# Performance work log

Measured on AMD Instinct MI355X. Metric: run time of the kernel, lower is better.

## Reference

```python
import jax, jax.numpy as jnp
import numpy as np

EPS = 1e-6        # eigenvalue clamp for numerical safety (matrices are well-conditioned by construction)
MOMENTUM = 0.1    # init kwarg


def _sym_apply(X, fn):
    """Apply a spectral function to a batch of symmetric matrices via eigh."""
    w, V = jnp.linalg.eigh(X)
    w = jnp.maximum(w, EPS)
    return jnp.einsum('...ij,...j,...kj->...ik', V, fn(w), V)


def sqrtm(X):
    return _sym_apply(X, jnp.sqrt)


def invsqrtm(X):
    return _sym_apply(X, lambda w: 1.0 / jnp.sqrt(w))


def logm(X):
    return _sym_apply(X, jnp.log)


def expm_sym(X):
    w, V = jnp.linalg.eigh(X)
    return jnp.einsum('...ij,...j,...kj->...ik', V, jnp.exp(w), V)


def powm(X, t):
    return _sym_apply(X, lambda w: w ** t)


def congr_neg(X, G):
    """CongrG(X, G, 'neg') = G^{-1/2} X G^{-1/2}, broadcast over batch dims of X."""
    Gi = invsqrtm(G)
    return jnp.einsum('ij,...jk,kl->...il', Gi, X, Gi)


def bary_geom(Xm):
    """Karcher (Frechet) mean of SPD matrices Xm: (N, n, n).
    One Karcher-flow step initialized at the arithmetic mean (SPDNet-BN convention)."""
    G = jnp.mean(Xm, axis=0)
    Gs, Gi = sqrtm(G), invsqrtm(G)
    L = logm(jnp.einsum('ij,bjk,kl->bil', Gi, Xm, Gi))   # log-maps at G
    return Gs @ expm_sym(jnp.mean(L, axis=0)) @ Gs


def geodesic(A, B, t):
    """SPD geodesic from A toward B at time t: A^{1/2} (A^{-1/2} B A^{-1/2})^t A^{1/2}."""
    As, Ai = sqrtm(A), invsqrtm(A)
    return As @ powm(Ai @ B @ Ai, t) @ As


def setup_inputs() -> dict:
    key = jax.random.key(0)
    N, T, V, M, n = 32, 64, 25, 2, 16
    A = jax.random.normal(key, (N, T, V, M, n, n), dtype=jnp.float32)
    # SPD construction: A A^T / n + 0.5 I  (min eigenvalue >= 0.5)
    X = jnp.einsum('...ij,...kj->...ik', A, A) / n + 0.5 * jnp.eye(n, dtype=jnp.float32)
    running_mean = jnp.eye(n, dtype=jnp.float32)  # torch.eye(n) in __init__
    return {"X": X, "running_mean": running_mean}


def reference(X, running_mean):
    N, T, V, M, n, _ = X.shape
    Xf = X.reshape(N, T * V * M, n, n)
    X_mean = jnp.mean(Xf, axis=1)                      # (N, n, n) per-sample arithmetic mean
    mean = bary_geom(X_mean)                           # (n, n) Karcher mean over batch
    new_running_mean = geodesic(running_mean, mean, MOMENTUM)  # no_grad EMA in torch
    X_centered = congr_neg(Xf, mean)                   # mean^{-1/2} X mean^{-1/2}
    return X_centered.reshape(N, T, V, M, n, n), new_running_mean
```

## Files before the change

kernel.cpp:

```cpp
#include <hip/hip_runtime.h>
#include <math.h>

#define NSAMP  32
#define BBATCH 3200
#define NMAT   102400
#define ST     20
#define IX(i,j) ((i)*ST+(j))
#define MSZ    (16*ST)

#define PART_O 0
#define WI_O   131072

#define NS_IT 5
#define LOG_M 7
#define EXP_M 6


__device__ __forceinline__ void wsync() {
  asm volatile("s_waitcnt lgkmcnt(0)" ::: "memory");
}

__device__ __forceinline__ void wmm(const float* A, const float* B, float* C, int l) {
  int i = l >> 2, j0 = (l & 3) << 2;
  float4 acc = make_float4(0.f, 0.f, 0.f, 0.f);
  #pragma unroll
  for (int k = 0; k < 16; ++k) {
    float a = A[IX(i, k)];
    const float4 b = *(const float4*)&B[IX(k, j0)];
    acc.x += a * b.x; acc.y += a * b.y; acc.z += a * b.z; acc.w += a * b.w;
  }
  *(float4*)&C[IX(i, j0)] = acc;
  wsync();
}

__device__ __forceinline__ void wmad_diag(float* C, float s, float d, int l) {
  int i = l >> 2, j0 = (l & 3) << 2;
  float4 p = *(float4*)&C[IX(i, j0)];
  p.x *= s; p.y *= s; p.z *= s; p.w *= s;
  if (i == j0) p.x += d; else if (i == j0 + 1) p.y += d;
  else if (i == j0 + 2) p.z += d; else if (i == j0 + 3) p.w += d;
  *(float4*)&C[IX(i, j0)] = p;
  wsync();
}

__device__ __forceinline__ void wset_I(float* C, float d, int l) {
  int i = l >> 2, j0 = (l & 3) << 2;
  float4 p = make_float4(0.f, 0.f, 0.f, 0.f);
  if (i == j0) p.x = d; else if (i == j0 + 1) p.y = d;
  else if (i == j0 + 2) p.z = d; else if (i == j0 + 3) p.w = d;
  *(float4*)&C[IX(i, j0)] = p;
  wsync();
}

__device__ __forceinline__ void wsym(float* A, int l) {
  int i = l >> 2, j0 = (l & 3) << 2;
  float4 a = *(float4*)&A[IX(i, j0)];
  float4 v;
  v.x = 0.5f * (a.x + A[IX(j0,     i)]);
  v.y = 0.5f * (a.y + A[IX(j0 + 1, i)]);
  v.z = 0.5f * (a.z + A[IX(j0 + 2, i)]);
  v.w = 0.5f * (a.w + A[IX(j0 + 3, i)]);
  wsync();
  *(float4*)&A[IX(i, j0)] = v;
  wsync();
}

__device__ __forceinline__ float wtrace(const float* A) {
  float tr = 0.f;
  #pragma unroll
  for (int k = 0; k < 16; ++k) tr += A[IX(k, k)];
  return tr;
}

__device__ __forceinline__ void wcpy(const float* src, float* dst, int l) {
  int i = l >> 2, j0 = (l & 3) << 2;
  *(float4*)&dst[IX(i, j0)] = *(const float4*)&src[IX(i, j0)];
  wsync();
}

__device__ void wns(float* Y0, float* Y1, float* Z0, float* Z1, float* P,
                    int l, float** pS, float** pZ) {
  float c = wtrace(Y0) * (1.f / 16.f);
  float ic = 1.f / c;
  int i = l >> 2, j0 = (l & 3) << 2;
  {
    float4 a = *(float4*)&Y0[IX(i, j0)];
    a.x *= ic; a.y *= ic; a.z *= ic; a.w *= ic;
    *(float4*)&Y0[IX(i, j0)] = a;
    float4 z = make_float4(0.f, 0.f, 0.f, 0.f);
    if (i == j0) z.x = 1.f; else if (i == j0 + 1) z.y = 1.f;
    else if (i == j0 + 2) z.z = 1.f; else if (i == j0 + 3) z.w = 1.f;
    *(float4*)&Z0[IX(i, j0)] = z;
  }
  wsync();
  float *Y = Y0, *Yn = Y1, *Z = Z0, *Zn = Z1;
  for (int it = 0; it < NS_IT; ++it) {
    wmm(Z, Y, P, l);
    wmad_diag(P, -0.5f, 1.5f, l);
    wmm(Y, P, Yn, l);
    wmm(P, Z, Zn, l);
    float* tp = Y; Y = Yn; Yn = tp;
    tp = Z; Z = Zn; Zn = tp;
  }
  float sc = sqrtf(c), isc = 1.f / sc;
  {
    float4 y = *(float4*)&Y[IX(i, j0)];
    y.x *= sc; y.y *= sc; y.z *= sc; y.w *= sc;
    *(float4*)&Y[IX(i, j0)] = y;
    float4 z = *(float4*)&Z[IX(i, j0)];
    z.x *= isc; z.y *= isc; z.z *= isc; z.w *= isc;
    *(float4*)&Z[IX(i, j0)] = z;
  }
  wsync();
  *pS = Y; *pZ = Z;
}

__device__ void wlog(float* S, float* L, float* R0, float* R1, int l) {
  wmad_diag(S, 1.f, -1.f, l);
  float am = ((LOG_M & 1) ? 1.f : -1.f) / (float)LOG_M;
  wset_I(R0, am, l);
  float *R = R0, *Rn = R1;
  for (int j = LOG_M - 1; j >= 1; --j) {
    wmm(S, R, Rn, l);
    float aj = ((j & 1) ? 1.f : -1.f) / (float)j;
    wmad_diag(Rn, 1.f, aj, l);
    float* tp = R; R = Rn; Rn = tp;
  }
  wmm(S, R, L, l);
}

__device__ float* wexp(const float* K, float* R0, float* R1, int l) {
  wset_I(R0, 1.f, l);
  float *R = R0, *Rn = R1;
  for (int j = EXP_M; j >= 1; --j) {
    wmm(K, R, Rn, l);
    wmad_diag(Rn, 1.f / (float)j, 1.f, l);
    float* tp = R; R = Rn; Rn = tp;
  }
  return R;
}


__global__ __launch_bounds__(512) void k_part(const float* __restrict__ X, float* __restrict__ ws) {
  int b = blockIdx.x >> 4;
  int c = blockIdx.x & 15;
  int t = threadIdx.x;
  int e4 = t & 63;
  int r  = t >> 6;
  const float4* X4 = (const float4*)X;
  float4 s = make_float4(0.f, 0.f, 0.f, 0.f);
  long mbase = (long)b * BBATCH + c * 200;
  for (int i = r; i < 200; i += 8) {
    float4 v = X4[(mbase + i) * 64 + e4];
    s.x += v.x; s.y += v.y; s.z += v.z; s.w += v.w;
  }
  __shared__ float4 red[512];
  red[t] = s;
  __syncthreads();
  if (t < 64) {
    float4 o = red[t];
    #pragma unroll
    for (int k = 1; k < 8; ++k) {
      float4 v = red[t + 64 * k];
      o.x += v.x; o.y += v.y; o.z += v.z; o.w += v.w;
    }
    ((float4*)(ws + PART_O))[(long)blockIdx.x * 64 + t] = o;
  }
}

__global__ __launch_bounds__(1024) void k_mid(const float* __restrict__ rm,
                                              float* __restrict__ ws,
                                              float* __restrict__ out) {
  __shared__ __align__(16) float XmL[NSAMP * 256];
  __shared__ __align__(16) float wb[16][4 * MSZ];
  __shared__ __align__(16) float GsL[MSZ], GiL[MSZ], RsL[MSZ], RiL[MSZ], meanL[MSZ];
  int t = threadIdx.x;
  int w = t >> 6, l = t & 63;

  for (int idx = t; idx < NSAMP * 256; idx += 1024) {
    int b = idx >> 8, e = idx & 255;
    float s = 0.f;
    #pragma unroll
    for (int c = 0; c < 16; ++c) s += ws[PART_O + (b * 16 + c) * 256 + e];
    XmL[idx] = s * (1.f / BBATCH);
  }
  __syncthreads();

  if (t < 256) {
    int i = t >> 4, j = t & 15;
    float s = 0.f;
    #pragma unroll
    for (int b = 0; b < NSAMP; ++b) s += XmL[b * 256 + t];
    wb[0][IX(i, j)] = s * (1.f / NSAMP);
  } else if (t < 512) {
    int e = t - 256, i = e >> 4, j = e & 15;
    wb[1][IX(i, j)] = rm[e];
  }
  __syncthreads();

  if (w == 0) {
    float *S, *Z;
    wns(&wb[0][0], &wb[0][MSZ], &wb[0][2*MSZ], &wb[0][3*MSZ], &wb[2][0], l, &S, &Z);
    wcpy(S, GsL, l); wcpy(Z, GiL, l);
  } else if (w == 1) {
    float *S, *Z;
    wns(&wb[1][0], &wb[1][MSZ], &wb[1][2*MSZ], &wb[1][3*MSZ], &wb[3][0], l, &S, &Z);
    wcpy(S, RsL, l); wcpy(Z, RiL, l);
  }
  __syncthreads();

  {
    float* B0 = &wb[w][0];       float* B1 = &wb[w][MSZ];
    float* B2 = &wb[w][2 * MSZ]; float* B3 = &wb[w][3 * MSZ];
    int i = l >> 2, j0 = (l & 3) << 2;
    for (int r = 0; r < 2; ++r) {
      int b = w + r * 16;
      *(float4*)&B0[IX(i, j0)] = *(const float4*)&XmL[b * 256 + i * 16 + j0];
      wsync();
      wmm(GiL, B0, B1, l);
      wmm(B1, GiL, B2, l);
      wsym(B2, l);
      wlog(B2, B3, B0, B1, l);
      *(float4*)&XmL[b * 256 + i * 16 + j0] = *(const float4*)&B3[IX(i, j0)];
      wsync();
    }
  }
  __syncthreads();

  if (t < 256) {
    int i = t >> 4, j = t & 15;
    float s = 0.f;
    #pragma unroll
    for (int b = 0; b < NSAMP; ++b) s += XmL[b * 256 + t];
    wb[0][IX(i, j)] = s * (1.f / NSAMP);
  }
  __syncthreads();
  if (w == 0) {
    float* E = wexp(&wb[0][0], &wb[0][MSZ], &wb[0][2 * MSZ], l);
    wmm(GsL, E, &wb[0][3 * MSZ], l);
    wmm(&wb[0][3 * MSZ], GsL, &wb[0][0], l);
    wsym(&wb[0][0], l);
    wcpy(&wb[0][0], meanL, l);
  }
  __syncthreads();

  if (w == 0) {
    wcpy(meanL, &wb[0][0], l);
    float *S, *Z;
    wns(&wb[0][0], &wb[0][MSZ], &wb[0][2*MSZ], &wb[0][3*MSZ], &wb[2][0], l, &S, &Z);
    int i = l >> 2, j0 = (l & 3) << 2;
    *(float4*)&ws[WI_O + i * 16 + j0] = *(const float4*)&Z[IX(i, j0)];
  } else if (w == 1) {
    float* b0 = &wb[1][0];       float* b1 = &wb[1][MSZ];
    float* b2 = &wb[1][2 * MSZ]; float* b3 = &wb[1][3 * MSZ];
    wmm(RiL, meanL, b0, l);
    wmm(b0, RiL, b1, l);
    wsym(b1, l);
    float c = wtrace(b1) * (1.f / 16.f);
    wmad_diag(b1, 1.f / c, 0.f, l);
    wlog(b1, b2, b0, b3, l);
    wmad_diag(b2, 0.1f, 0.f, l);
    float* E = wexp(b2, b0, b3, l);
    float s = expf(0.1f * logf(c));
    wmad_diag(E, s, 0.f, l);
    wmm(RsL, E, b1, l);
    wmm(b1, RsL, b3, l);
    int i = l >> 2, j0 = (l & 3) << 2;
    *(float4*)&out[(size_t)NMAT * 256 + i * 16 + j0] = *(const float4*)&b3[IX(i, j0)];
  }
}

__global__ __launch_bounds__(256) void k_center(const float* __restrict__ X,
                                                const float* __restrict__ ws,
                                                float* __restrict__ out) {
  __shared__ __align__(16) float Wsm[MSZ];
  __shared__ __align__(16) float Xs[4 * MSZ];
  __shared__ __align__(16) float Ts[4 * MSZ];
  int t = threadIdx.x;
  long m0 = (long)blockIdx.x * 4;
  Wsm[(t >> 4) * ST + (t & 15)] = ws[WI_O + t];
  const float4* X4 = (const float4*)X;
  float4 xv = X4[m0 * 64 + t];
  int mw = t >> 6;
  int l  = t & 63;
  int i  = l >> 2;
  int j0 = (l & 3) << 2;
  *(float4*)&Xs[mw * MSZ + i * ST + j0] = xv;
  __syncthreads();
  float4 a = make_float4(0.f, 0.f, 0.f, 0.f);
  #pragma unroll
  for (int k = 0; k < 16; ++k) {
    float x = Xs[mw * MSZ + i * ST + k];
    const float4 wv = *(const float4*)&Wsm[k * ST + j0];
    a.x += x * wv.x; a.y += x * wv.y; a.z += x * wv.z; a.w += x * wv.w;
  }
  *(float4*)&Ts[mw * MSZ + i * ST + j0] = a;
  wsync();
  float4 y = make_float4(0.f, 0.f, 0.f, 0.f);
  #pragma unroll
  for (int k = 0; k < 16; ++k) {
    float w = Wsm[i * ST + k];
    const float4 tv = *(const float4*)&Ts[mw * MSZ + k * ST + j0];
    y.x += w * tv.x; y.y += w * tv.y; y.z += w * tv.z; y.w += w * tv.w;
  }
  ((float4*)out)[m0 * 64 + t] = y;
}

extern "C" void kernel_launch(void* const* d_in, const int* in_sizes, int n_in,
                              void* d_out, int out_size, void* d_ws, size_t ws_size,
                              hipStream_t stream) {
  (void)in_sizes; (void)n_in; (void)out_size; (void)ws_size;
  const float* X  = (const float*)d_in[0];
  const float* rm = (const float*)d_in[1];
  float* out = (float*)d_out;
  float* ws  = (float*)d_ws;

  k_part   <<<dim3(512),   dim3(512),  0, stream>>>(X, ws);
  k_mid    <<<dim3(1),     dim3(1024), 0, stream>>>(rm, ws, out);
  k_center <<<dim3(25600), dim3(256),  0, stream>>>(X, ws, out);
}
```

Measured before the change: 247.4 us.

## Persist W in registers, loop 8 rounds per block, use DPP for second GEMM

The centering kernel now processes 32 matrices per block over 8 rounds instead of 4, keeping the whitening matrix and its rows in registers rather than reloading from LDS. The next matrix is prefetched from global memory while the current one is computed. The second multiply uses DPP quad broadcasts instead of an LDS round-trip through a temporary buffer, and outputs use nontemporal stores. This cuts LDS traffic, launch count and per-block setup in a memory-bound kernel, at the cost of higher register pressure and fewer blocks.

```diff
diff --git a/kernel.cpp b/kernel.cpp
--- a/kernel.cpp
+++ b/kernel.cpp
@@ -14,6 +14,8 @@
 #define NS_IT 5
 #define LOG_M 7
 #define EXP_M 6
+
+typedef float nf4 __attribute__((ext_vector_type(4)));
 
 
 __device__ __forceinline__ void wsync() {
@@ -138,6 +140,12 @@
     float* tp = R; R = Rn; Rn = tp;
   }
   return R;
+}
+
+template<int Q>
+__device__ __forceinline__ float qb(float v) {
+  return __int_as_float(__builtin_amdgcn_mov_dpp(
+      __float_as_int(v), (Q | (Q << 2) | (Q << 4) | (Q << 6)), 0xF, 0xF, true));
 }
 
 
@@ -270,40 +278,52 @@
   }
 }
 
+#define ROUNDS 8
 __global__ __launch_bounds__(256) void k_center(const float* __restrict__ X,
                                                 const float* __restrict__ ws,
                                                 float* __restrict__ out) {
   __shared__ __align__(16) float Wsm[MSZ];
   __shared__ __align__(16) float Xs[4 * MSZ];
-  __shared__ __align__(16) float Ts[4 * MSZ];
   int t = threadIdx.x;
-  long m0 = (long)blockIdx.x * 4;
+  int mw = t >> 6, l = t & 63;
+  int i = l >> 2, j0 = (l & 3) << 2;
   Wsm[(t >> 4) * ST + (t & 15)] = ws[WI_O + t];
-  const float4* X4 = (const float4*)X;
-  float4 xv = X4[m0 * 64 + t];
-  int mw = t >> 6;
-  int l  = t & 63;
-  int i  = l >> 2;
-  int j0 = (l & 3) << 2;
-  *(float4*)&Xs[mw * MSZ + i * ST + j0] = xv;
-  __syncthreads();
-  float4 a = make_float4(0.f, 0.f, 0.f, 0.f);
+  __syncthreads();
+  float4 w4[16];
+  float  wr[16];
   #pragma unroll
   for (int k = 0; k < 16; ++k) {
-    float x = Xs[mw * MSZ + i * ST + k];
-    const float4 wv = *(const float4*)&Wsm[k * ST + j0];
-    a.x += x * wv.x; a.y += x * wv.y; a.z += x * wv.z; a.w += x * wv.w;
-  }
-  *(float4*)&Ts[mw * MSZ + i * ST + j0] = a;
-  wsync();
-  float4 y = make_float4(0.f, 0.f, 0.f, 0.f);
+    w4[k] = *(const float4*)&Wsm[IX(k, j0)];
+    wr[k] = Wsm[IX(i, k)];
+  }
+  const float4* X4 = (const float4*)X;
+  nf4* O4 = (nf4*)out;
+  long gi = ((long)blockIdx.x * (4 * ROUNDS) + mw) * 64 + l;
+  float4 xv = X4[gi];
   #pragma unroll
-  for (int k = 0; k < 16; ++k) {
-    float w = Wsm[i * ST + k];
-    const float4 tv = *(const float4*)&Ts[mw * MSZ + k * ST + j0];
-    y.x += w * tv.x; y.y += w * tv.y; y.z += w * tv.z; y.w += w * tv.w;
-  }
-  ((float4*)out)[m0 * 64 + t] = y;
+  for (int r = 0; r < ROUNDS; ++r) {
+    *(float4*)&Xs[mw * MSZ + IX(i, j0)] = xv;
+    if (r + 1 < ROUNDS) xv = X4[gi + 256 * (r + 1)];
+    wsync();
+    float4 tt = make_float4(0.f, 0.f, 0.f, 0.f);
+    #pragma unroll
+    for (int k = 0; k < 16; ++k) {
+      const float4 xk = *(const float4*)&Xs[mw * MSZ + IX(k, j0)];
+      tt.x += wr[k] * xk.x; tt.y += wr[k] * xk.y;
+      tt.z += wr[k] * xk.z; tt.w += wr[k] * xk.w;
+    }
+    float4 y = make_float4(0.f, 0.f, 0.f, 0.f);
+    #define PH2(Q) { \
+      float c0 = qb<Q>(tt.x), c1 = qb<Q>(tt.y), c2 = qb<Q>(tt.z), c3 = qb<Q>(tt.w); \
+      y.x += c0*w4[4*Q+0].x + c1*w4[4*Q+1].x + c2*w4[4*Q+2].x + c3*w4[4*Q+3].x; \
+      y.y += c0*w4[4*Q+0].y + c1*w4[4*Q+1].y + c2*w4[4*Q+2].y + c3*w4[4*Q+3].y; \
+      y.z += c0*w4[4*Q+0].z + c1*w4[4*Q+1].z + c2*w4[4*Q+2].z + c3*w4[4*Q+3].z; \
+      y.w += c0*w4[4*Q+0].w + c1*w4[4*Q+1].w + c2*w4[4*Q+2].w + c3*w4[4*Q+3].w; }
+    PH2(0) PH2(1) PH2(2) PH2(3)
+    #undef PH2
+    nf4 yv; yv.x = y.x; yv.y = y.y; yv.z = y.z; yv.w = y.w;
+    __builtin_nontemporal_store(yv, &O4[gi + 256 * r]);
+  }
 }
 
 extern "C" void kernel_launch(void* const* d_in, const int* in_sizes, int n_in,
@@ -315,7 +335,7 @@
   float* out = (float*)d_out;
   float* ws  = (float*)d_ws;
 
-  k_part   <<<dim3(512),   dim3(512),  0, stream>>>(X, ws);
-  k_mid    <<<dim3(1),     dim3(1024), 0, stream>>>(rm, ws, out);
-  k_center <<<dim3(25600), dim3(256),  0, stream>>>(X, ws, out);
-}
+  k_part   <<<dim3(512),  dim3(512),  0, stream>>>(X, ws);
+  k_mid    <<<dim3(1),    dim3(1024), 0, stream>>>(rm, ws, out);
+  k_center <<<dim3(3200), dim3(256),  0, stream>>>(X, ws, out);
+}
```

New measurement: 246.4 us. Within noise of the previous version (-0.4%).
